# Performance work log

Hardware: AMD Instinct MI355X
Metric: run time of the kernel (lower is better)

Reference implementation:

```python
import jax, jax.numpy as jnp
import numpy as np

# OCR letter geometry: img dim 128 -> 16x8 pixel letters (special-case in source)
LETTER_H, LETTER_W = 16, 8
OUT_CHANNELS = 1


def setup_inputs() -> dict:
    key = jax.random.key(0)
    kx, kk = jax.random.split(key)
    x = jax.random.normal(kx, (512, 512, 128), dtype=jnp.float32)
    kernel = jax.random.normal(kk, (3, 3), dtype=jnp.float32)
    return {"x": x, "kernel": kernel}


def reference(x, kernel):
    # x: (B, S, 128) -> letters of (16, 8); VALID conv with single 3x3 kernel,
    # stride 1, flattened per letter, replicated across out_channels.
    B, S, img = x.shape
    kH, kW = kernel.shape
    Ho, Wo = LETTER_H - kH + 1, LETTER_W - kW + 1  # 14, 6
    lhs = x.reshape(B * S, 1, LETTER_H, LETTER_W)          # NCHW
    rhs = kernel.reshape(1, 1, kH, kW)                     # OIHW
    out = jax.lax.conv_general_dilated(lhs, rhs, window_strides=(1, 1), padding="VALID")
    out = out.reshape(B, S, Ho * Wo)                       # (B, S, 84)
    # (out_channels, B, S, out_dim); same kernel for every out channel
    return jnp.broadcast_to(out[None], (OUT_CHANNELS, B, S, Ho * Wo))
```

## Files before the change

### kernel.cpp

```cpp
#include <hip/hip_runtime.h>

#define BLOCK 256
#define LETTERS_PER_BLOCK 64
#define LETTER_SZ 128
#define OUT_PER_LETTER 84
#define OUT_PER_BLOCK (LETTERS_PER_BLOCK * OUT_PER_LETTER)
#define IN_FLOATS_PER_BLOCK (LETTERS_PER_BLOCK * LETTER_SZ)

__global__ __launch_bounds__(BLOCK) void conv_letters_kernel(
    const float* __restrict__ x,
    const float* __restrict__ kern,
    float* __restrict__ out)
{
    __shared__ float s[IN_FLOATS_PER_BLOCK];

    const int t = threadIdx.x;
    const long long blk = blockIdx.x;

    const float4* in4 = reinterpret_cast<const float4*>(x) + blk * (IN_FLOATS_PER_BLOCK / 4);
    float4* s4 = reinterpret_cast<float4*>(s);
    #pragma unroll
    for (int i = 0; i < IN_FLOATS_PER_BLOCK / 4 / BLOCK; ++i) {
        s4[t + i * BLOCK] = in4[t + i * BLOCK];
    }

    const float k0 = kern[0], k1 = kern[1], k2 = kern[2];
    const float k3 = kern[3], k4 = kern[4], k5 = kern[5];
    const float k6 = kern[6], k7 = kern[7], k8 = kern[8];

    __syncthreads();

    float* outb = out + blk * (long long)OUT_PER_BLOCK;
    #pragma unroll
    for (int i = 0; i < OUT_PER_BLOCK / BLOCK; ++i) {
        const int oidx   = t + i * BLOCK;
        const int letter = oidx / OUT_PER_LETTER;
        const int within = oidx - letter * OUT_PER_LETTER;
        const int ho     = within / 6;
        const int wo     = within - ho * 6;
        const float* p = s + letter * LETTER_SZ + ho * 8 + wo;
        const float acc =
              k0 * p[0]  + k1 * p[1]  + k2 * p[2]
            + k3 * p[8]  + k4 * p[9]  + k5 * p[10]
            + k6 * p[16] + k7 * p[17] + k8 * p[18];
        outb[oidx] = acc;
    }
}

extern "C" void kernel_launch(void* const* d_in, const int* in_sizes, int n_in,
                              void* d_out, int out_size, void* d_ws, size_t ws_size,
                              hipStream_t stream) {
    const float* x    = (const float*)d_in[0];
    const float* kern = (const float*)d_in[1];
    float* out = (float*)d_out;

    const int total_letters = in_sizes[0] / LETTER_SZ;
    const int grid = total_letters / LETTERS_PER_BLOCK;

    conv_letters_kernel<<<grid, BLOCK, 0, stream>>>(x, kern, out);
}
```

Measured before the change: 40.53 us.

## Compute conv with register row windows, stage output in LDS, vector nontemporal stores

```diff
diff --git a/kernel.cpp b/kernel.cpp
--- a/kernel.cpp
+++ b/kernel.cpp
@@ -1,27 +1,32 @@
 #include <hip/hip_runtime.h>
 
+typedef float f4 __attribute__((ext_vector_type(4)));
+typedef float f2 __attribute__((ext_vector_type(2)));
+
 #define BLOCK 256
-#define LETTERS_PER_BLOCK 64
+#define LPB 64
 #define LETTER_SZ 128
+#define IN_FLOATS (LPB * LETTER_SZ)
 #define OUT_PER_LETTER 84
-#define OUT_PER_BLOCK (LETTERS_PER_BLOCK * OUT_PER_LETTER)
-#define IN_FLOATS_PER_BLOCK (LETTERS_PER_BLOCK * LETTER_SZ)
+#define OUT_FLOATS (LPB * OUT_PER_LETTER)
 
 __global__ __launch_bounds__(BLOCK) void conv_letters_kernel(
     const float* __restrict__ x,
     const float* __restrict__ kern,
     float* __restrict__ out)
 {
-    __shared__ float s[IN_FLOATS_PER_BLOCK];
+    __shared__ float s[IN_FLOATS + OUT_FLOATS];
 
     const int t = threadIdx.x;
     const long long blk = blockIdx.x;
 
-    const float4* in4 = reinterpret_cast<const float4*>(x) + blk * (IN_FLOATS_PER_BLOCK / 4);
-    float4* s4 = reinterpret_cast<float4*>(s);
+    const f4* in4 = reinterpret_cast<const f4*>(x) + blk * (IN_FLOATS / 4);
     #pragma unroll
-    for (int i = 0; i < IN_FLOATS_PER_BLOCK / 4 / BLOCK; ++i) {
-        s4[t + i * BLOCK] = in4[t + i * BLOCK];
+    for (int i = 0; i < IN_FLOATS / 4 / BLOCK; ++i) {
+        const int j = t + i * BLOCK;
+        const int fidx = 4 * j;
+        const int sidx = fidx ^ (((fidx >> 7) & 7) << 2);
+        *reinterpret_cast<f4*>(s + sidx) = __builtin_nontemporal_load(in4 + j);
     }
 
     const float k0 = kern[0], k1 = kern[1], k2 = kern[2];
@@ -30,20 +35,57 @@
 
     __syncthreads();
 
-    float* outb = out + blk * (long long)OUT_PER_BLOCK;
+    if (t < 2 * LPB) {
+        const int l = t >> 1;
+        const int h = t & 1;
+        const int sw = (l & 7) << 2;
+        const int base = l * LETTER_SZ + h * 56;
+        float* so = s + IN_FLOATS + t * 42;
+
+        float w[3][8];
+
+#define LOADROW(slot, ridx) do {                                            \
+            const int f0_ = base + (ridx) * 8;                              \
+            const f4 a_ = *reinterpret_cast<const f4*>(s + ( f0_      ^ sw)); \
+            const f4 b_ = *reinterpret_cast<const f4*>(s + ((f0_ + 4) ^ sw)); \
+            w[slot][0]=a_.x; w[slot][1]=a_.y; w[slot][2]=a_.z; w[slot][3]=a_.w; \
+            w[slot][4]=b_.x; w[slot][5]=b_.y; w[slot][6]=b_.z; w[slot][7]=b_.w; \
+        } while (0)
+
+        LOADROW(0, 0);
+        LOADROW(1, 1);
+
+        #pragma unroll
+        for (int orow = 0; orow < 7; ++orow) {
+            const int R0 = orow % 3;
+            const int R1 = (orow + 1) % 3;
+            const int R2 = (orow + 2) % 3;
+            LOADROW(R2, orow + 2);
+
+            #pragma unroll
+            for (int oc = 0; oc < 6; oc += 2) {
+                f2 v;
+                v.x = k0 * w[R0][oc]     + k1 * w[R0][oc + 1] + k2 * w[R0][oc + 2]
+                    + k3 * w[R1][oc]     + k4 * w[R1][oc + 1] + k5 * w[R1][oc + 2]
+                    + k6 * w[R2][oc]     + k7 * w[R2][oc + 1] + k8 * w[R2][oc + 2];
+                v.y = k0 * w[R0][oc + 1] + k1 * w[R0][oc + 2] + k2 * w[R0][oc + 3]
+                    + k3 * w[R1][oc + 1] + k4 * w[R1][oc + 2] + k5 * w[R1][oc + 3]
+                    + k6 * w[R2][oc + 1] + k7 * w[R2][oc + 2] + k8 * w[R2][oc + 3];
+                *reinterpret_cast<f2*>(so + orow * 6 + oc) = v;
+            }
+        }
+#undef LOADROW
+    }
+
+    __syncthreads();
+
+    f4* ob = reinterpret_cast<f4*>(out + blk * (long long)OUT_FLOATS);
+    const f4* so4 = reinterpret_cast<const f4*>(s + IN_FLOATS);
     #pragma unroll
-    for (int i = 0; i < OUT_PER_BLOCK / BLOCK; ++i) {
-        const int oidx   = t + i * BLOCK;
-        const int letter = oidx / OUT_PER_LETTER;
-        const int within = oidx - letter * OUT_PER_LETTER;
-        const int ho     = within / 6;
-        const int wo     = within - ho * 6;
-        const float* p = s + letter * LETTER_SZ + ho * 8 + wo;
-        const float acc =
-              k0 * p[0]  + k1 * p[1]  + k2 * p[2]
-            + k3 * p[8]  + k4 * p[9]  + k5 * p[10]
-            + k6 * p[16] + k7 * p[17] + k8 * p[18];
-        outb[oidx] = acc;
+    for (int i = 0; i < 6; ++i) {
+        const int idx = t + i * BLOCK;
+        if (idx < OUT_FLOATS / 4)
+            __builtin_nontemporal_store(so4[idx], ob + idx);
     }
 }
 
@@ -55,7 +97,7 @@
     float* out = (float*)d_out;
 
     const int total_letters = in_sizes[0] / LETTER_SZ;
-    const int grid = total_letters / LETTERS_PER_BLOCK;
+    const int grid = total_letters / LPB;
 
     conv_letters_kernel<<<grid, BLOCK, 0, stream>>>(x, kern, out);
 }
```

Result: no change. 40.30 us (-0.6%).

## Give each wavefront its own LDS slab, drop block barrier, vectorize stores

Applied to the files above, without the earlier changes.

```diff
diff --git a/kernel.cpp b/kernel.cpp
--- a/kernel.cpp
+++ b/kernel.cpp
@@ -1,50 +1,74 @@
 #include <hip/hip_runtime.h>
 
+typedef float f4 __attribute__((ext_vector_type(4)));
+
 #define BLOCK 256
-#define LETTERS_PER_BLOCK 64
+#define LPW 16
 #define LETTER_SZ 128
-#define OUT_PER_LETTER 84
-#define OUT_PER_BLOCK (LETTERS_PER_BLOCK * OUT_PER_LETTER)
-#define IN_FLOATS_PER_BLOCK (LETTERS_PER_BLOCK * LETTER_SZ)
+#define IN_FLOATS_W (LPW * LETTER_SZ)
+#define OPL 84
+#define OUT_FLOATS_W (LPW * OPL)
+#define LETTERS_PER_BLOCK (4 * LPW)
 
 __global__ __launch_bounds__(BLOCK) void conv_letters_kernel(
     const float* __restrict__ x,
     const float* __restrict__ kern,
     float* __restrict__ out)
 {
-    __shared__ float s[IN_FLOATS_PER_BLOCK];
+    __shared__ float s[4 * IN_FLOATS_W];
 
     const int t = threadIdx.x;
-    const long long blk = blockIdx.x;
+    const int w = t >> 6;
+    const int lane = t & 63;
+    float* slab = s + w * IN_FLOATS_W;
 
-    const float4* in4 = reinterpret_cast<const float4*>(x) + blk * (IN_FLOATS_PER_BLOCK / 4);
-    float4* s4 = reinterpret_cast<float4*>(s);
+    const long long l0 = (long long)blockIdx.x * LETTERS_PER_BLOCK + w * LPW;
+
+    const f4* in4 = reinterpret_cast<const f4*>(x) + l0 * (LETTER_SZ / 4);
     #pragma unroll
-    for (int i = 0; i < IN_FLOATS_PER_BLOCK / 4 / BLOCK; ++i) {
-        s4[t + i * BLOCK] = in4[t + i * BLOCK];
+    for (int i = 0; i < IN_FLOATS_W / 4 / 64; ++i) {
+        const int j = lane + i * 64;
+        *reinterpret_cast<f4*>(slab + 4 * j) = __builtin_nontemporal_load(in4 + j);
     }
 
     const float k0 = kern[0], k1 = kern[1], k2 = kern[2];
     const float k3 = kern[3], k4 = kern[4], k5 = kern[5];
     const float k6 = kern[6], k7 = kern[7], k8 = kern[8];
 
-    __syncthreads();
+    asm volatile("s_waitcnt lgkmcnt(0)" ::: "memory");
+    __builtin_amdgcn_sched_barrier(0);
 
-    float* outb = out + blk * (long long)OUT_PER_BLOCK;
+    float acc[21];
     #pragma unroll
-    for (int i = 0; i < OUT_PER_BLOCK / BLOCK; ++i) {
-        const int oidx   = t + i * BLOCK;
-        const int letter = oidx / OUT_PER_LETTER;
-        const int within = oidx - letter * OUT_PER_LETTER;
+    for (int i = 0; i < 21; ++i) {
+        const int oidx   = lane + i * 64;
+        const int letter = oidx / OPL;
+        const int within = oidx - letter * OPL;
         const int ho     = within / 6;
         const int wo     = within - ho * 6;
-        const float* p = s + letter * LETTER_SZ + ho * 8 + wo;
-        const float acc =
-              k0 * p[0]  + k1 * p[1]  + k2 * p[2]
-            + k3 * p[8]  + k4 * p[9]  + k5 * p[10]
-            + k6 * p[16] + k7 * p[17] + k8 * p[18];
-        outb[oidx] = acc;
+        const float* p = slab + letter * LETTER_SZ + ho * 8 + wo;
+        acc[i] = k0 * p[0]  + k1 * p[1]  + k2 * p[2]
+               + k3 * p[8]  + k4 * p[9]  + k5 * p[10]
+               + k6 * p[16] + k7 * p[17] + k8 * p[18];
     }
+
+    asm volatile("s_waitcnt lgkmcnt(0)" ::: "memory");
+    __builtin_amdgcn_sched_barrier(0);
+
+    #pragma unroll
+    for (int i = 0; i < 21; ++i)
+        slab[lane + i * 64] = acc[i];
+
+    asm volatile("s_waitcnt lgkmcnt(0)" ::: "memory");
+    __builtin_amdgcn_sched_barrier(0);
+
+    f4* ob = reinterpret_cast<f4*>(out + l0 * OPL);
+    const f4* so4 = reinterpret_cast<const f4*>(slab);
+    #pragma unroll
+    for (int i = 0; i < 5; ++i)
+        __builtin_nontemporal_store(so4[lane + i * 64], ob + lane + i * 64);
+    if (lane < 16)
+        __builtin_nontemporal_store(so4[lane + 320], ob + lane + 320);
 }
 
 extern "C" void kernel_launch(void* const* d_in, const int* in_sizes, int n_in,
```

Result: slower. 41.98 us (+3.6%).

## Stream letter slabs per wave with async LDS double buffering

Applied to the files above, without the earlier changes.

```diff
diff --git a/kernel.cpp b/kernel.cpp
--- a/kernel.cpp
+++ b/kernel.cpp
@@ -1,49 +1,76 @@
 #include <hip/hip_runtime.h>
 
+
 #define BLOCK 256
-#define LETTERS_PER_BLOCK 64
+#define LPW 16
 #define LETTER_SZ 128
-#define OUT_PER_LETTER 84
-#define OUT_PER_BLOCK (LETTERS_PER_BLOCK * OUT_PER_LETTER)
-#define IN_FLOATS_PER_BLOCK (LETTERS_PER_BLOCK * LETTER_SZ)
+#define SLAB_FLOATS (LPW * LETTER_SZ)
+#define OPL 84
+#define OUT_PER_SLAB (LPW * OPL)
+#define SLABS_PER_WAVE 8
+
+__device__ __forceinline__ void dma16(const float* g, float* l) {
+    __builtin_amdgcn_global_load_lds(
+        (const __attribute__((address_space(1))) void*)g,
+        (__attribute__((address_space(3))) void*)l, 16, 0, 0);
+}
 
 __global__ __launch_bounds__(BLOCK) void conv_letters_kernel(
     const float* __restrict__ x,
     const float* __restrict__ kern,
     float* __restrict__ out)
 {
-    __shared__ float s[IN_FLOATS_PER_BLOCK];
+    __shared__ float s[4 * 2 * SLAB_FLOATS];
 
     const int t = threadIdx.x;
-    const long long blk = blockIdx.x;
+    const int w = t >> 6;
+    const int lane = t & 63;
+    float* lds = s + w * 2 * SLAB_FLOATS;
 
-    const float4* in4 = reinterpret_cast<const float4*>(x) + blk * (IN_FLOATS_PER_BLOCK / 4);
-    float4* s4 = reinterpret_cast<float4*>(s);
-    #pragma unroll
-    for (int i = 0; i < IN_FLOATS_PER_BLOCK / 4 / BLOCK; ++i) {
-        s4[t + i * BLOCK] = in4[t + i * BLOCK];
-    }
+    const int wid = blockIdx.x * 4 + w;
+    const float* gbase = x + (size_t)wid * SLABS_PER_WAVE * SLAB_FLOATS;
+    float* obase = out + (size_t)wid * SLABS_PER_WAVE * OUT_PER_SLAB;
 
     const float k0 = kern[0], k1 = kern[1], k2 = kern[2];
     const float k3 = kern[3], k4 = kern[4], k5 = kern[5];
     const float k6 = kern[6], k7 = kern[7], k8 = kern[8];
 
-    __syncthreads();
+    #pragma unroll
+    for (int i = 0; i < 8; ++i)
+        dma16(gbase + (size_t)(i * 64 + lane) * 4, lds + i * 256);
 
-    float* outb = out + blk * (long long)OUT_PER_BLOCK;
-    #pragma unroll
-    for (int i = 0; i < OUT_PER_BLOCK / BLOCK; ++i) {
-        const int oidx   = t + i * BLOCK;
-        const int letter = oidx / OUT_PER_LETTER;
-        const int within = oidx - letter * OUT_PER_LETTER;
-        const int ho     = within / 6;
-        const int wo     = within - ho * 6;
-        const float* p = s + letter * LETTER_SZ + ho * 8 + wo;
-        const float acc =
-              k0 * p[0]  + k1 * p[1]  + k2 * p[2]
-            + k3 * p[8]  + k4 * p[9]  + k5 * p[10]
-            + k6 * p[16] + k7 * p[17] + k8 * p[18];
-        outb[oidx] = acc;
+    #pragma unroll 1
+    for (int k = 0; k < SLABS_PER_WAVE; ++k) {
+        const float* cur = lds + (k & 1) * SLAB_FLOATS;
+
+        if (k + 1 < SLABS_PER_WAVE) {
+            const float* gn = gbase + (size_t)(k + 1) * SLAB_FLOATS;
+            float* nxt = lds + ((k + 1) & 1) * SLAB_FLOATS;
+            #pragma unroll
+            for (int i = 0; i < 8; ++i)
+                dma16(gn + (size_t)(i * 64 + lane) * 4, nxt + i * 256);
+        }
+
+        if (k == 0)                         { asm volatile("s_waitcnt vmcnt(8)"  ::: "memory"); }
+        else if (k + 1 < SLABS_PER_WAVE)    { asm volatile("s_waitcnt vmcnt(29)" ::: "memory"); }
+        else                                { asm volatile("s_waitcnt vmcnt(21)" ::: "memory"); }
+        __builtin_amdgcn_sched_barrier(0);
+
+        float* outk = obase + (size_t)k * OUT_PER_SLAB;
+        #pragma unroll
+        for (int i = 0; i < 21; ++i) {
+            const int oidx   = lane + i * 64;
+            const int letter = oidx / OPL;
+            const int within = oidx - letter * OPL;
+            const int ho     = within / 6;
+            const int wo     = within - ho * 6;
+            const float* p = cur + letter * LETTER_SZ + ho * 8 + wo;
+            const float acc =
+                  k0 * p[0]  + k1 * p[1]  + k2 * p[2]
+                + k3 * p[8]  + k4 * p[9]  + k5 * p[10]
+                + k6 * p[16] + k7 * p[17] + k8 * p[18];
+            __builtin_nontemporal_store(acc, outk + oidx);
+        }
     }
 }
 
@@ -55,7 +82,7 @@
     float* out = (float*)d_out;
 
     const int total_letters = in_sizes[0] / LETTER_SZ;
-    const int grid = total_letters / LETTERS_PER_BLOCK;
+    const int grid = total_letters / (LPW * SLABS_PER_WAVE * 4);
 
     conv_letters_kernel<<<grid, BLOCK, 0, stream>>>(x, kern, out);
 }
```

Result: slower. 41.42 us (+2.2%).
